# Optimization experiments

Hardware: AMD Instinct MI355X
Metric: run time of the kernel (lower is better)

## Reference

```python
import jax, jax.numpy as jnp
import numpy as np

VOCAB = 50257
D_EMB = 1024
N_NODES = 4096

def setup_inputs() -> dict:
    key = jax.random.key(0)
    k1, k2, k3 = jax.random.split(key, 3)
    x = jax.random.normal(k1, (N_NODES, D_EMB), dtype=jnp.float32)
    W = jax.random.normal(k2, (VOCAB, D_EMB), dtype=jnp.float32) * 0.02
    y = jax.random.randint(k3, (N_NODES,), 0, VOCAB, dtype=jnp.int64)
    return {"x": x, "W": W, "y": y}

def reference(x, W, y):
    # Decoder: logits = x @ W.T  -> (n_nodes, vocab)
    logits = jnp.einsum('nd,vd->nv', x, W)
    # CrossEntropyLoss (mean reduction)
    logp = jax.nn.log_softmax(logits, axis=-1)
    nll = -jnp.take_along_axis(logp, y[:, None], axis=-1)[:, 0]
    return jnp.mean(nll)
```

## Files before the change

kernel.cpp:

```cpp
#include <hip/hip_runtime.h>
#include <hip/hip_bf16.h>
#include <math.h>


#define N_NODES 4096
#define D_EMB   1024
#define VOCAB   50257
#define VPAD    50432
#define NT      197
#define KT      16

typedef __attribute__((ext_vector_type(8))) short short8;
typedef __attribute__((ext_vector_type(4))) float f32x4;

__device__ __forceinline__ unsigned short f2bf(float f) {
  unsigned int x = __float_as_uint(f);
  x += 0x7fffu + ((x >> 16) & 1u);
  return (unsigned short)(x >> 16);
}

__global__ void cvt_w_kernel(const float* __restrict__ W, unsigned short* __restrict__ Wb) {
  long long gid = (long long)blockIdx.x * 256 + threadIdx.x;
  long long e = gid << 3;
  int row = (int)(e >> 10);
  short8 o;
  if (row < VOCAB) {
    const float4* p = (const float4*)(W + e);
    float4 u = p[0];
    float4 v = p[1];
    o[0] = (short)f2bf(u.x); o[1] = (short)f2bf(u.y); o[2] = (short)f2bf(u.z); o[3] = (short)f2bf(u.w);
    o[4] = (short)f2bf(v.x); o[5] = (short)f2bf(v.y); o[6] = (short)f2bf(v.z); o[7] = (short)f2bf(v.w);
  } else {
    o[0]=0; o[1]=0; o[2]=0; o[3]=0; o[4]=0; o[5]=0; o[6]=0; o[7]=0;
  }
  *(short8*)(Wb + e) = o;
}

__global__ void cvt_x_kernel(const float* __restrict__ x, unsigned short* __restrict__ Xb) {
  long long gid = (long long)blockIdx.x * 256 + threadIdx.x;
  long long e = gid << 3;
  const float4* p = (const float4*)(x + e);
  float4 u = p[0];
  float4 v = p[1];
  short8 o;
  o[0] = (short)f2bf(u.x); o[1] = (short)f2bf(u.y); o[2] = (short)f2bf(u.z); o[3] = (short)f2bf(u.w);
  o[4] = (short)f2bf(v.x); o[5] = (short)f2bf(v.y); o[6] = (short)f2bf(v.z); o[7] = (short)f2bf(v.w);
  *(short8*)(Xb + e) = o;
}

__global__ void dot_y_kernel(const float* __restrict__ x, const float* __restrict__ W,
                             const int* __restrict__ y, float* __restrict__ logit_y) {
  __shared__ float red[4];
  const int n = blockIdx.x;
  const int t = threadIdx.x;
  const int lbl = y[n];
  const float* xr = x + ((long long)n << 10);
  const float* wr = W + ((long long)lbl << 10);
  float s = 0.f;
  #pragma unroll
  for (int i = 0; i < 4; ++i) {
    int k = t + i * 256;
    s = fmaf(xr[k], wr[k], s);
  }
  #pragma unroll
  for (int m = 32; m; m >>= 1) s += __shfl_xor(s, m, 64);
  if ((t & 63) == 0) red[t >> 6] = s;
  __syncthreads();
  if (t == 0) logit_y[n] = red[0] + red[1] + red[2] + red[3];
}

#define MFMAQ(Q, AF)                                                                  \
  do {                                                                                \
    _Pragma("unroll")                                                                 \
    for (int ni = 0; ni < 4; ++ni) {                                                  \
      _Pragma("unroll")                                                               \
      for (int kk = 0; kk < 2; ++kk) {                                                \
        acc[2*(Q)  ][ni] = __builtin_amdgcn_mfma_f32_16x16x32_bf16(AF[0][kk], bf[ni][kk], acc[2*(Q)  ][ni], 0, 0, 0); \
        acc[2*(Q)+1][ni] = __builtin_amdgcn_mfma_f32_16x16x32_bf16(AF[1][kk], bf[ni][kk], acc[2*(Q)+1][ni], 0, 0, 0); \
      }                                                                               \
    }                                                                                 \
  } while (0)

#define STAGE(U)                                                                      \
  do {                                                                                \
    const int _b = (U) & 1;                                                           \
    const long long _ko = (long long)(U) * 64;                                        \
    _Pragma("unroll")                                                                 \
    for (int h = 0; h < 2; ++h) {                                                     \
      _Pragma("unroll")                                                               \
      for (int p = 0; p < 2; ++p) {                                                   \
        __builtin_amdgcn_global_load_lds(                                             \
            (const __attribute__((address_space(1))) void*)(Xb + abase[h][p] + _ko),  \
            (__attribute__((address_space(3))) void*)(sh + _b*32768 + h*8192 + p*4096 + dst0), \
            16, 0, 0);                                                                \
      }                                                                               \
    }                                                                                 \
    _Pragma("unroll")                                                                 \
    for (int h = 0; h < 2; ++h) {                                                     \
      _Pragma("unroll")                                                               \
      for (int p = 0; p < 2; ++p) {                                                   \
        __builtin_amdgcn_global_load_lds(                                             \
            (const __attribute__((address_space(1))) void*)(Wb + bbase[h][p] + _ko),  \
            (__attribute__((address_space(3))) void*)(sh + _b*32768 + 16384 + h*8192 + p*4096 + dst0), \
            16, 0, 0);                                                                \
      }                                                                               \
    }                                                                                 \
  } while (0)

__global__ __launch_bounds__(512, 2) void gemm_stats_kernel(
    const unsigned short* __restrict__ Xb,
    const unsigned short* __restrict__ Wb,
    float2* __restrict__ partials)
{
  __shared__ __align__(16) unsigned short sh[65536];

  const int tid  = threadIdx.x;
  const int lane = tid & 63;
  const int wid  = tid >> 6;
  const int wr   = wid >> 2;
  const int wcol = wid & 3;
  const int g    = lane >> 4;
  const int r16  = lane & 15;

  const int bm0 = blockIdx.x * 256;
  const int bn0 = blockIdx.y * 256;

  const int srb = tid >> 3;
  const int scg = ((tid & 7) << 3) ^ ((srb & 7) << 3);
  const int dst0 = tid * 8;
  long long abase[2][2], bbase[2][2];
  #pragma unroll
  for (int h = 0; h < 2; ++h)
    #pragma unroll
    for (int p = 0; p < 2; ++p) {
      abase[h][p] = (long long)(bm0 + h*128 + p*64 + srb) * D_EMB + scg;
      bbase[h][p] = (long long)(bn0 + h*128 + p*64 + srb) * D_EMB + scg;
    }

  f32x4 acc[8][4];
  #pragma unroll
  for (int m = 0; m < 8; ++m)
    #pragma unroll
    for (int n = 0; n < 4; ++n)
      #pragma unroll
      for (int j = 0; j < 4; ++j)
        acc[m][n][j] = 0.f;

  const int arow = wr * 128 + r16;
  const int brow = wcol * 64 + r16;
  const int sw   = (r16 & 7) << 3;
  const int colp0 = (g * 8) ^ sw;
  const int colp1 = (32 + g * 8) ^ sw;

  STAGE(0);
  STAGE(1);
  asm volatile("s_waitcnt vmcnt(8)" ::: "memory");
  __builtin_amdgcn_s_barrier();

  for (int u = 0; u < KT; ++u) {
    const unsigned short* Ab = sh + (u & 1) * 32768;
    const unsigned short* Bb = Ab + 16384;

    short8 bf[4][2], aA[2][2], aB[2][2];
    #pragma unroll
    for (int ni = 0; ni < 4; ++ni) {
      bf[ni][0] = *(const short8*)(Bb + (brow + ni*16)*64 + colp0);
      bf[ni][1] = *(const short8*)(Bb + (brow + ni*16)*64 + colp1);
    }
    #pragma unroll
    for (int i = 0; i < 2; ++i) {
      aA[i][0] = *(const short8*)(Ab + (arow + i*16)*64 + colp0);
      aA[i][1] = *(const short8*)(Ab + (arow + i*16)*64 + colp1);
      aB[i][0] = *(const short8*)(Ab + (arow + (2+i)*16)*64 + colp0);
      aB[i][1] = *(const short8*)(Ab + (arow + (2+i)*16)*64 + colp1);
    }

    __builtin_amdgcn_s_setprio(1);
    MFMAQ(0, aA);
    __builtin_amdgcn_s_setprio(0);

    #pragma unroll
    for (int i = 0; i < 2; ++i) {
      aA[i][0] = *(const short8*)(Ab + (arow + (4+i)*16)*64 + colp0);
      aA[i][1] = *(const short8*)(Ab + (arow + (4+i)*16)*64 + colp1);
    }
    __builtin_amdgcn_s_setprio(1);
    MFMAQ(1, aB);
    __builtin_amdgcn_s_setprio(0);

    #pragma unroll
    for (int i = 0; i < 2; ++i) {
      aB[i][0] = *(const short8*)(Ab + (arow + (6+i)*16)*64 + colp0);
      aB[i][1] = *(const short8*)(Ab + (arow + (6+i)*16)*64 + colp1);
    }
    __builtin_amdgcn_s_setprio(1);
    MFMAQ(2, aA);
    __builtin_amdgcn_s_setprio(0);

    asm volatile("s_waitcnt lgkmcnt(0)" ::: "memory");
    __builtin_amdgcn_s_barrier();

    if (u < KT - 2) STAGE(u + 2);

    __builtin_amdgcn_s_setprio(1);
    MFMAQ(3, aB);
    __builtin_amdgcn_s_setprio(0);

    if (u < KT - 2) {
      asm volatile("s_waitcnt vmcnt(8)" ::: "memory");
      __builtin_amdgcn_s_barrier();
    } else if (u == KT - 2) {
      asm volatile("s_waitcnt vmcnt(0)" ::: "memory");
      __builtin_amdgcn_s_barrier();
    }
  }

  float2 (*stats)[4] = (float2 (*)[4])sh;
  #pragma unroll
  for (int mi = 0; mi < 8; ++mi) {
    #pragma unroll
    for (int j = 0; j < 4; ++j) {
      float vmax = -INFINITY;
      #pragma unroll
      for (int ni = 0; ni < 4; ++ni) {
        const int colg = bn0 + wcol*64 + ni*16 + r16;
        float v = (colg < VOCAB) ? acc[mi][ni][j] : -INFINITY;
        vmax = fmaxf(vmax, v);
      }
      vmax = fmaxf(vmax, __shfl_xor(vmax, 1));
      vmax = fmaxf(vmax, __shfl_xor(vmax, 2));
      vmax = fmaxf(vmax, __shfl_xor(vmax, 4));
      vmax = fmaxf(vmax, __shfl_xor(vmax, 8));
      float ssum = 0.f;
      #pragma unroll
      for (int ni = 0; ni < 4; ++ni) {
        const int colg = bn0 + wcol*64 + ni*16 + r16;
        if (colg < VOCAB) ssum += __expf(acc[mi][ni][j] - vmax);
      }
      ssum += __shfl_xor(ssum, 1);
      ssum += __shfl_xor(ssum, 2);
      ssum += __shfl_xor(ssum, 4);
      ssum += __shfl_xor(ssum, 8);
      if (r16 == 0) {
        stats[wr*128 + mi*16 + g*4 + j][wcol] = make_float2(vmax, ssum);
      }
    }
  }
  __syncthreads();
  if (tid < 256) {
    float2 a0 = stats[tid][0], a1 = stats[tid][1], a2 = stats[tid][2], a3 = stats[tid][3];
    float M = fmaxf(fmaxf(a0.x, a1.x), fmaxf(a2.x, a3.x));
    float S = a0.y * __expf(a0.x - M) + a1.y * __expf(a1.x - M)
            + a2.y * __expf(a2.x - M) + a3.y * __expf(a3.x - M);
    partials[(long long)(bm0 + tid) * NT + blockIdx.y] = make_float2(M, S);
  }
}

__global__ void lse_kernel(const float2* __restrict__ partials,
                           const float* __restrict__ logit_y,
                           float* __restrict__ row_nll) {
  const int n = blockIdx.x * 4 + (threadIdx.x >> 6);
  const int l = threadIdx.x & 63;
  const float2* pr = partials + (long long)n * NT;
  float M = -INFINITY, S = 0.f;
  for (int t = l; t < NT; t += 64) {
    float2 p = pr[t];
    float nM = fmaxf(M, p.x);
    S = S * __expf(M - nM) + p.y * __expf(p.x - nM);
    M = nM;
  }
  #pragma unroll
  for (int off = 1; off < 64; off <<= 1) {
    float Mo = __shfl_xor(M, off);
    float So = __shfl_xor(S, off);
    float nM = fmaxf(M, Mo);
    S = S * __expf(M - nM) + So * __expf(Mo - nM);
    M = nM;
  }
  if (l == 0) row_nll[n] = (M + logf(S)) - logit_y[n];
}

__global__ void mean_kernel(const float* __restrict__ row_nll, float* __restrict__ out) {
  __shared__ float red[4];
  float s = 0.f;
  for (int i = threadIdx.x; i < N_NODES; i += 256) s += row_nll[i];
  #pragma unroll
  for (int m = 32; m; m >>= 1) s += __shfl_xor(s, m, 64);
  if ((threadIdx.x & 63) == 0) red[threadIdx.x >> 6] = s;
  __syncthreads();
  if (threadIdx.x == 0) out[0] = (red[0] + red[1] + red[2] + red[3]) * (1.0f / N_NODES);
}

extern "C" void kernel_launch(void* const* d_in, const int* in_sizes, int n_in,
                              void* d_out, int out_size, void* d_ws, size_t ws_size,
                              hipStream_t stream) {
  const float* x = (const float*)d_in[0];
  const float* W = (const float*)d_in[1];
  const int*   y = (const int*)d_in[2];
  float* out = (float*)d_out;

  char* ws = (char*)d_ws;
  unsigned short* Wb = (unsigned short*)ws;
  unsigned short* Xb = (unsigned short*)(ws + 103284736);
  float2* partials   = (float2*)(ws + 111673344);
  float* logit_y     = (float*)(ws + 118128640);
  float* row_nll     = (float*)(ws + 118145024);

  hipLaunchKernelGGL(cvt_w_kernel, dim3(VPAD * (D_EMB / 8) / 256), dim3(256), 0, stream, W, Wb);
  hipLaunchKernelGGL(cvt_x_kernel, dim3(N_NODES * (D_EMB / 8) / 256), dim3(256), 0, stream, x, Xb);
  hipLaunchKernelGGL(dot_y_kernel, dim3(N_NODES), dim3(256), 0, stream, x, W, y, logit_y);
  hipLaunchKernelGGL(gemm_stats_kernel, dim3(16, NT), dim3(512), 0, stream, Xb, Wb, partials);
  hipLaunchKernelGGL(lse_kernel, dim3(N_NODES / 4), dim3(256), 0, stream, partials, logit_y, row_nll);
  hipLaunchKernelGGL(mean_kernel, dim3(1), dim3(256), 0, stream, row_nll, out);
}
```

Measured before the change: 803.6 us.

## Interleave GEMM prefetch across MFMA phases, fuse label dot into LSE, grid-stride W convert

The GEMM main loop is rebuilt so the next K-tile's global-to-LDS loads are split into small chunks issued between the four MFMA quarter-phases. Each phase is bracketed by barriers and priority changes, and the vmcnt wait is tightened. The separate label-logit dot kernel is removed and its dot product is computed inside the LSE kernel, saving a launch and a pass over x. The W conversion kernel becomes a grid-stride loop with a fixed 2048-block grid. The extra barriers per phase add synchronisation cost, and the finer load split changes how much latency is hidden.

```diff
diff --git a/kernel.cpp b/kernel.cpp
--- a/kernel.cpp
+++ b/kernel.cpp
@@ -20,20 +20,23 @@
 }
 
 __global__ void cvt_w_kernel(const float* __restrict__ W, unsigned short* __restrict__ Wb) {
-  long long gid = (long long)blockIdx.x * 256 + threadIdx.x;
-  long long e = gid << 3;
-  int row = (int)(e >> 10);
-  short8 o;
-  if (row < VOCAB) {
-    const float4* p = (const float4*)(W + e);
-    float4 u = p[0];
-    float4 v = p[1];
-    o[0] = (short)f2bf(u.x); o[1] = (short)f2bf(u.y); o[2] = (short)f2bf(u.z); o[3] = (short)f2bf(u.w);
-    o[4] = (short)f2bf(v.x); o[5] = (short)f2bf(v.y); o[6] = (short)f2bf(v.z); o[7] = (short)f2bf(v.w);
-  } else {
-    o[0]=0; o[1]=0; o[2]=0; o[3]=0; o[4]=0; o[5]=0; o[6]=0; o[7]=0;
-  }
-  *(short8*)(Wb + e) = o;
+  const long long total = (long long)VPAD * (D_EMB / 8);
+  for (long long gid = (long long)blockIdx.x * 256 + threadIdx.x; gid < total;
+       gid += (long long)gridDim.x * 256) {
+    long long e = gid << 3;
+    int row = (int)(e >> 10);
+    short8 o;
+    if (row < VOCAB) {
+      const float4* p = (const float4*)(W + e);
+      float4 u = p[0];
+      float4 v = p[1];
+      o[0] = (short)f2bf(u.x); o[1] = (short)f2bf(u.y); o[2] = (short)f2bf(u.z); o[3] = (short)f2bf(u.w);
+      o[4] = (short)f2bf(v.x); o[5] = (short)f2bf(v.y); o[6] = (short)f2bf(v.z); o[7] = (short)f2bf(v.w);
+    } else {
+      o[0]=0; o[1]=0; o[2]=0; o[3]=0; o[4]=0; o[5]=0; o[6]=0; o[7]=0;
+    }
+    *(short8*)(Wb + e) = o;
+  }
 }
 
 __global__ void cvt_x_kernel(const float* __restrict__ x, unsigned short* __restrict__ Xb) {
@@ -48,64 +51,49 @@
   *(short8*)(Xb + e) = o;
 }
 
-__global__ void dot_y_kernel(const float* __restrict__ x, const float* __restrict__ W,
-                             const int* __restrict__ y, float* __restrict__ logit_y) {
-  __shared__ float red[4];
-  const int n = blockIdx.x;
-  const int t = threadIdx.x;
-  const int lbl = y[n];
-  const float* xr = x + ((long long)n << 10);
-  const float* wr = W + ((long long)lbl << 10);
-  float s = 0.f;
-  #pragma unroll
-  for (int i = 0; i < 4; ++i) {
-    int k = t + i * 256;
-    s = fmaf(xr[k], wr[k], s);
-  }
-  #pragma unroll
-  for (int m = 32; m; m >>= 1) s += __shfl_xor(s, m, 64);
-  if ((t & 63) == 0) red[t >> 6] = s;
-  __syncthreads();
-  if (t == 0) logit_y[n] = red[0] + red[1] + red[2] + red[3];
-}
-
-#define MFMAQ(Q, AF)                                                                  \
+#define MFMAQ(Q)                                                                      \
   do {                                                                                \
     _Pragma("unroll")                                                                 \
     for (int ni = 0; ni < 4; ++ni) {                                                  \
       _Pragma("unroll")                                                               \
       for (int kk = 0; kk < 2; ++kk) {                                                \
-        acc[2*(Q)  ][ni] = __builtin_amdgcn_mfma_f32_16x16x32_bf16(AF[0][kk], bf[ni][kk], acc[2*(Q)  ][ni], 0, 0, 0); \
-        acc[2*(Q)+1][ni] = __builtin_amdgcn_mfma_f32_16x16x32_bf16(AF[1][kk], bf[ni][kk], acc[2*(Q)+1][ni], 0, 0, 0); \
+        acc[2*(Q)  ][ni] = __builtin_amdgcn_mfma_f32_16x16x32_bf16(af[0][kk], bf[ni][kk], acc[2*(Q)  ][ni], 0, 0, 0); \
+        acc[2*(Q)+1][ni] = __builtin_amdgcn_mfma_f32_16x16x32_bf16(af[1][kk], bf[ni][kk], acc[2*(Q)+1][ni], 0, 0, 0); \
       }                                                                               \
     }                                                                                 \
   } while (0)
 
-#define STAGE(U)                                                                      \
-  do {                                                                                \
-    const int _b = (U) & 1;                                                           \
-    const long long _ko = (long long)(U) * 64;                                        \
-    _Pragma("unroll")                                                                 \
-    for (int h = 0; h < 2; ++h) {                                                     \
-      _Pragma("unroll")                                                               \
-      for (int p = 0; p < 2; ++p) {                                                   \
-        __builtin_amdgcn_global_load_lds(                                             \
-            (const __attribute__((address_space(1))) void*)(Xb + abase[h][p] + _ko),  \
-            (__attribute__((address_space(3))) void*)(sh + _b*32768 + h*8192 + p*4096 + dst0), \
-            16, 0, 0);                                                                \
-      }                                                                               \
-    }                                                                                 \
-    _Pragma("unroll")                                                                 \
-    for (int h = 0; h < 2; ++h) {                                                     \
-      _Pragma("unroll")                                                               \
-      for (int p = 0; p < 2; ++p) {                                                   \
-        __builtin_amdgcn_global_load_lds(                                             \
-            (const __attribute__((address_space(1))) void*)(Wb + bbase[h][p] + _ko),  \
-            (__attribute__((address_space(3))) void*)(sh + _b*32768 + 16384 + h*8192 + p*4096 + dst0), \
-            16, 0, 0);                                                                \
-      }                                                                               \
-    }                                                                                 \
+#define STAGE_A(U, P)                                                                 \
+  do {                                                                               \
+    const int _b = (U) & 1;                                                          \
+    const long long _ko = (long long)(U) * 64;                                       \
+    _Pragma("unroll")                                                                \
+    for (int h = 0; h < 2; ++h)                                                      \
+      __builtin_amdgcn_global_load_lds(                                              \
+          (const __attribute__((address_space(1))) void*)(Xb + abase[h][P] + _ko),   \
+          (__attribute__((address_space(3))) void*)(sh + _b*32768 + h*8192 + (P)*4096 + dst0), \
+          16, 0, 0);                                                                 \
   } while (0)
+#define STAGE_B(U, P)                                                                 \
+  do {                                                                               \
+    const int _b = (U) & 1;                                                          \
+    const long long _ko = (long long)(U) * 64;                                       \
+    _Pragma("unroll")                                                                \
+    for (int h = 0; h < 2; ++h)                                                      \
+      __builtin_amdgcn_global_load_lds(                                              \
+          (const __attribute__((address_space(1))) void*)(Wb + bbase[h][P] + _ko),   \
+          (__attribute__((address_space(3))) void*)(sh + _b*32768 + 16384 + h*8192 + (P)*4096 + dst0), \
+          16, 0, 0);                                                                 \
+  } while (0)
+
+#define PHASE_OPEN()                                   \
+  __builtin_amdgcn_s_barrier();                        \
+  asm volatile("s_waitcnt lgkmcnt(0)" ::: "memory");   \
+  __builtin_amdgcn_sched_barrier(0);                   \
+  __builtin_amdgcn_s_setprio(1)
+#define PHASE_CLOSE()                                  \
+  __builtin_amdgcn_s_setprio(0);                       \
+  __builtin_amdgcn_s_barrier()
 
 __global__ __launch_bounds__(512, 2) void gemm_stats_kernel(
     const unsigned short* __restrict__ Xb,
@@ -152,16 +140,16 @@
   const int colp0 = (g * 8) ^ sw;
   const int colp1 = (32 + g * 8) ^ sw;
 
-  STAGE(0);
-  STAGE(1);
-  asm volatile("s_waitcnt vmcnt(8)" ::: "memory");
+  STAGE_A(0, 0); STAGE_A(0, 1); STAGE_B(0, 0); STAGE_B(0, 1);
+  STAGE_A(1, 0);
+  asm volatile("s_waitcnt vmcnt(2)" ::: "memory");
   __builtin_amdgcn_s_barrier();
 
   for (int u = 0; u < KT; ++u) {
     const unsigned short* Ab = sh + (u & 1) * 32768;
     const unsigned short* Bb = Ab + 16384;
-
-    short8 bf[4][2], aA[2][2], aB[2][2];
+    short8 bf[4][2], af[2][2];
+
     #pragma unroll
     for (int ni = 0; ni < 4; ++ni) {
       bf[ni][0] = *(const short8*)(Bb + (brow + ni*16)*64 + colp0);
@@ -169,45 +157,48 @@
     }
     #pragma unroll
     for (int i = 0; i < 2; ++i) {
-      aA[i][0] = *(const short8*)(Ab + (arow + i*16)*64 + colp0);
-      aA[i][1] = *(const short8*)(Ab + (arow + i*16)*64 + colp1);
-      aB[i][0] = *(const short8*)(Ab + (arow + (2+i)*16)*64 + colp0);
-      aB[i][1] = *(const short8*)(Ab + (arow + (2+i)*16)*64 + colp1);
-    }
-
+      af[i][0] = *(const short8*)(Ab + (arow + i*16)*64 + colp0);
+      af[i][1] = *(const short8*)(Ab + (arow + i*16)*64 + colp1);
+    }
+    if (u + 1 < KT) STAGE_A(u + 1, 1);
+    PHASE_OPEN();
+    MFMAQ(0);
+    PHASE_CLOSE();
+
+    #pragma unroll
+    for (int i = 0; i < 2; ++i) {
+      af[i][0] = *(const short8*)(Ab + (arow + (2+i)*16)*64 + colp0);
+      af[i][1] = *(const short8*)(Ab + (arow + (2+i)*16)*64 + colp1);
+    }
+    if (u + 1 < KT) STAGE_B(u + 1, 0);
+    PHASE_OPEN();
+    MFMAQ(1);
+    PHASE_CLOSE();
+
+    #pragma unroll
+    for (int i = 0; i < 2; ++i) {
+      af[i][0] = *(const short8*)(Ab + (arow + (4+i)*16)*64 + colp0);
+      af[i][1] = *(const short8*)(Ab + (arow + (4+i)*16)*64 + colp1);
+    }
+    if (u + 1 < KT) STAGE_B(u + 1, 1);
+    if (u + 2 < KT) STAGE_A(u + 2, 0);
+    PHASE_OPEN();
+    MFMAQ(2);
+    PHASE_CLOSE();
+
+    #pragma unroll
+    for (int i = 0; i < 2; ++i) {
+      af[i][0] = *(const short8*)(Ab + (arow + (6+i)*16)*64 + colp0);
+      af[i][1] = *(const short8*)(Ab + (arow + (6+i)*16)*64 + colp1);
+    }
+    __builtin_amdgcn_s_barrier();
+    asm volatile("s_waitcnt lgkmcnt(0)" ::: "memory");
+    __builtin_amdgcn_sched_barrier(0);
     __builtin_amdgcn_s_setprio(1);
-    MFMAQ(0, aA);
+    MFMAQ(3);
     __builtin_amdgcn_s_setprio(0);
-
-    #pragma unroll
-    for (int i = 0; i < 2; ++i) {
-      aA[i][0] = *(const short8*)(Ab + (arow + (4+i)*16)*64 + colp0);
-      aA[i][1] = *(const short8*)(Ab + (arow + (4+i)*16)*64 + colp1);
-    }
-    __builtin_amdgcn_s_setprio(1);
-    MFMAQ(1, aB);
-    __builtin_amdgcn_s_setprio(0);
-
-    #pragma unroll
-    for (int i = 0; i < 2; ++i) {
-      aB[i][0] = *(const short8*)(Ab + (arow + (6+i)*16)*64 + colp0);
-      aB[i][1] = *(const short8*)(Ab + (arow + (6+i)*16)*64 + colp1);
-    }
-    __builtin_amdgcn_s_setprio(1);
-    MFMAQ(2, aA);
-    __builtin_amdgcn_s_setprio(0);
-
-    asm volatile("s_waitcnt lgkmcnt(0)" ::: "memory");
-    __builtin_amdgcn_s_barrier();
-
-    if (u < KT - 2) STAGE(u + 2);
-
-    __builtin_amdgcn_s_setprio(1);
-    MFMAQ(3, aB);
-    __builtin_amdgcn_s_setprio(0);
-
     if (u < KT - 2) {
-      asm volatile("s_waitcnt vmcnt(8)" ::: "memory");
+      asm volatile("s_waitcnt vmcnt(2)" ::: "memory");
       __builtin_amdgcn_s_barrier();
     } else if (u == KT - 2) {
       asm volatile("s_waitcnt vmcnt(0)" ::: "memory");
@@ -257,7 +248,9 @@
 }
 
 __global__ void lse_kernel(const float2* __restrict__ partials,
-                           const float* __restrict__ logit_y,
+                           const float* __restrict__ x,
+                           const float* __restrict__ W,
+                           const int* __restrict__ y,
                            float* __restrict__ row_nll) {
   const int n = blockIdx.x * 4 + (threadIdx.x >> 6);
   const int l = threadIdx.x & 63;
@@ -269,6 +262,15 @@
     S = S * __expf(M - nM) + p.y * __expf(p.x - nM);
     M = nM;
   }
+  const float4* xr = (const float4*)(x + ((long long)n << 10));
+  const float4* wv = (const float4*)(W + ((long long)y[n] << 10));
+  float dot = 0.f;
+  #pragma unroll
+  for (int i = 0; i < 4; ++i) {
+    float4 a = xr[l + 64*i];
+    float4 b = wv[l + 64*i];
+    dot = fmaf(a.x, b.x, fmaf(a.y, b.y, fmaf(a.z, b.z, fmaf(a.w, b.w, dot))));
+  }
   #pragma unroll
   for (int off = 1; off < 64; off <<= 1) {
     float Mo = __shfl_xor(M, off);
@@ -276,8 +278,9 @@
     float nM = fmaxf(M, Mo);
     S = S * __expf(M - nM) + So * __expf(Mo - nM);
     M = nM;
-  }
-  if (l == 0) row_nll[n] = (M + logf(S)) - logit_y[n];
+    dot += __shfl_xor(dot, off);
+  }
+  if (l == 0) row_nll[n] = (M + logf(S)) - dot;
 }
 
 __global__ void mean_kernel(const float* __restrict__ row_nll, float* __restrict__ out) {
@@ -305,11 +308,11 @@
   float2* partials   = (float2*)(ws + 111673344);
   float* logit_y     = (float*)(ws + 118128640);
   float* row_nll     = (float*)(ws + 118145024);
-
-  hipLaunchKernelGGL(cvt_w_kernel, dim3(VPAD * (D_EMB / 8) / 256), dim3(256), 0, stream, W, Wb);
+  (void)logit_y;
+
+  hipLaunchKernelGGL(cvt_w_kernel, dim3(2048), dim3(256), 0, stream, W, Wb);
   hipLaunchKernelGGL(cvt_x_kernel, dim3(N_NODES * (D_EMB / 8) / 256), dim3(256), 0, stream, x, Xb);
-  hipLaunchKernelGGL(dot_y_kernel, dim3(N_NODES), dim3(256), 0, stream, x, W, y, logit_y);
   hipLaunchKernelGGL(gemm_stats_kernel, dim3(16, NT), dim3(512), 0, stream, Xb, Wb, partials);
-  hipLaunchKernelGGL(lse_kernel, dim3(N_NODES / 4), dim3(256), 0, stream, partials, logit_y, row_nll);
+  hipLaunchKernelGGL(lse_kernel, dim3(N_NODES / 4), dim3(256), 0, stream, partials, x, W, y, row_nll);
   hipLaunchKernelGGL(mean_kernel, dim3(1), dim3(256), 0, stream, row_nll, out);
 }
```

Measured after the change: 796.7 us. No clear change (-0.9%).
